# Performance work log

Hardware: AMD Instinct MI355X
Metric: run time of the kernel (lower is better)

The kernel has to match this reference:

```python
import jax, jax.numpy as jnp
from jax import lax
import numpy as np

NPOINT, K, EPS = 2048, 16, 1e-5


def fps(xyz, npoint):
    # Farthest point sampling. Deterministic start index 0 (torch uses randint).
    B, N, _ = xyz.shape
    def step(carry, _):
        distance, far = carry
        centroid = jnp.take_along_axis(xyz, far[:, None, None], axis=1)  # [B,1,3]
        d = jnp.sum((xyz - centroid) ** 2, axis=-1)                      # [B,N]
        distance = jnp.minimum(distance, d)
        return (distance, jnp.argmax(distance, axis=-1)), far
    init = (jnp.full((B, N), 1e10, dtype=xyz.dtype), jnp.zeros((B,), jnp.int32))
    _, cent = lax.scan(step, init, None, length=npoint)  # [npoint, B]
    return jnp.transpose(cent)  # [B, npoint]


def gather(points, idx):
    # points [B,N,C], idx [B,...] -> [B,...,C]
    return jax.vmap(lambda p, i: p[i])(points, idx)


def bn_relu(x, gamma, beta):
    # x [B,S,K,C]; BatchNorm2d training-mode stats over (B,S,K) per channel
    mu = jnp.mean(x, axis=(0, 1, 2), keepdims=True)
    var = jnp.var(x, axis=(0, 1, 2), keepdims=True)
    return jax.nn.relu((x - mu) * lax.rsqrt(var + EPS) * gamma + beta)


def setup_inputs() -> dict:
    key = jax.random.key(0)
    ks = jax.random.split(key, 8)
    B, N, C_in, C_out = 4, 8192, 64, 128
    return {
        'xyz': jax.random.normal(ks[0], (B, N, 3), jnp.float32),
        'feat': jax.random.normal(ks[1], (B, N, C_in), jnp.float32),
        'W1': jax.random.normal(ks[2], (C_in + 3, C_out), jnp.float32) * 0.05,
        'g1': jnp.ones((C_out,), jnp.float32),
        'b1': jnp.zeros((C_out,), jnp.float32),
        'W2': jax.random.normal(ks[3], (C_out, C_out), jnp.float32) * 0.05,
        'g2': jnp.ones((C_out,), jnp.float32),
        'b2': jnp.zeros((C_out,), jnp.float32),
    }


def reference(xyz, feat, W1, g1, b1, W2, g2, b2):
    fps_idx = fps(xyz, NPOINT)
    new_xyz = gather(xyz, fps_idx)                              # [B,S,3]
    # squared distances [B,S,N] via ||a||^2 + ||b||^2 - 2 a.b (avoids [B,S,N,3])
    d = (jnp.sum(new_xyz ** 2, -1)[:, :, None]
         + jnp.sum(xyz ** 2, -1)[:, None, :]
         - 2.0 * jnp.einsum('bsc,bnc->bsn', new_xyz, xyz))
    _, idx = lax.top_k(-d, K)                                   # [B,S,K] smallest dists
    g_xyz = gather(xyz, idx)                                    # [B,S,K,3]
    g_feat = gather(feat, idx)                                  # [B,S,K,C]
    x = jnp.concatenate([g_feat, g_xyz - new_xyz[:, :, None]], axis=-1)
    x = bn_relu(jnp.einsum('bskc,co->bsko', x, W1), g1, b1)     # 1x1 conv == matmul
    x = bn_relu(jnp.einsum('bskc,co->bsko', x, W2), g2, b2)
    new_feat = jnp.max(x, axis=2)                               # max over K -> [B,S,Cout]
    return new_xyz, new_feat
```

## Files before the change

kernel.cpp:

```cpp
#include <hip/hip_runtime.h>
#include <hip/hip_bf16.h>

#define N_PTS 8192
#define N_SAMP 2048
#define KNN_K 16
#define NBATCH 4
#define BN_M (NBATCH * N_SAMP * KNN_K)
#define NROWS (N_SAMP * NBATCH * KNN_K)
#define KNN_WAVES 2016
#define CHUNK 64

typedef float f32x2 __attribute__((ext_vector_type(2)));

template <int CTRL, int RM>
__device__ __forceinline__ unsigned umax_dpp(unsigned v) {
  unsigned o = (unsigned)__builtin_amdgcn_update_dpp((int)v, (int)v, CTRL, RM, 0xF, false);
  return (o > v) ? o : v;
}

__global__ __launch_bounds__(512) void fused_fps_knn(
    const float* __restrict__ xyz, float* __restrict__ new_xyz,
    int* __restrict__ knn_idx, int* __restrict__ progress) {
#pragma clang fp contract(off)
  __shared__ __align__(16) float xyzw[N_PTS * 4];
  __shared__ unsigned redbuf[8];
  __shared__ unsigned winslot[2];
  __shared__ int sampwin[CHUNK];
  const int tid = threadIdx.x;
  const int lane = tid & 63;

  if (blockIdx.x < NBATCH) {
    const int b = blockIdx.x;
    const int wid = tid >> 6;
    const float* base = xyz + (size_t)b * N_PTS * 3;
    for (int i = tid; i < N_PTS * 3; i += 512) {
      float v = base[i];
      int p = i / 3, c = i - p * 3;
      xyzw[p * 4 + c] = v;
    }
    for (int i = tid; i < N_PTS; i += 512) xyzw[i * 4 + 3] = 0.f;
    if (tid == 0) { winslot[0] = 0u; winslot[1] = 0xFFFFFFFFu; }
    __syncthreads();

    f32x2 px[8], py[8], pz[8], dmin[8];
#pragma unroll
    for (int j = 0; j < 8; ++j) {
      int p0 = (2 * j) * 512 + tid, p1 = p0 + 512;
      const float4 a = *reinterpret_cast<const float4*>(&xyzw[p0 * 4]);
      const float4 c = *reinterpret_cast<const float4*>(&xyzw[p1 * 4]);
      px[j] = f32x2{a.x, c.x};
      py[j] = f32x2{a.y, c.y};
      pz[j] = f32x2{a.z, c.z};
      dmin[j] = f32x2{1e10f, 1e10f};
    }
    for (int it = 1; it < N_SAMP; ++it) {
      const int p = it & 1;
      const unsigned cur = winslot[p ^ 1];
      if (tid == 0) sampwin[(it - 1) & (CHUNK - 1)] = (int)cur;
      const bool pub = (it & (CHUNK - 1)) == 0;
      if (pub && tid < CHUNK) {
        const int idx = (tid == CHUNK - 1) ? (int)cur : sampwin[tid];
        const float4 c4 = *reinterpret_cast<const float4*>(&xyzw[idx * 4]);
        float* dst = new_xyz + ((size_t)b * N_SAMP + (it - CHUNK) + tid) * 3;
        dst[0] = c4.x; dst[1] = c4.y; dst[2] = c4.z;
      }
      const float4 c4 = *reinterpret_cast<const float4*>(&xyzw[cur * 4]);
      f32x2 cX = {c4.x, c4.x}, cY = {c4.y, c4.y}, cZ = {c4.z, c4.z};
#pragma unroll
      for (int j = 0; j < 8; ++j) {
        f32x2 dx = px[j] - cX;
        f32x2 dy = py[j] - cY;
        f32x2 dz = pz[j] - cZ;
        f32x2 s01 = dx * dx + dy * dy;
        f32x2 d = s01 + dz * dz;
        dmin[j].x = fminf(dmin[j].x, d.x);
        dmin[j].y = fminf(dmin[j].y, d.y);
      }
      f32x2 m0 = {fmaxf(dmin[0].x, dmin[1].x), fmaxf(dmin[0].y, dmin[1].y)};
      f32x2 m1 = {fmaxf(dmin[2].x, dmin[3].x), fmaxf(dmin[2].y, dmin[3].y)};
      f32x2 m2 = {fmaxf(dmin[4].x, dmin[5].x), fmaxf(dmin[4].y, dmin[5].y)};
      f32x2 m3 = {fmaxf(dmin[6].x, dmin[7].x), fmaxf(dmin[6].y, dmin[7].y)};
      f32x2 n0 = {fmaxf(m0.x, m1.x), fmaxf(m0.y, m1.y)};
      f32x2 n1 = {fmaxf(m2.x, m3.x), fmaxf(m2.y, m3.y)};
      f32x2 nn = {fmaxf(n0.x, n1.x), fmaxf(n0.y, n1.y)};
      const unsigned bd = __float_as_uint(fmaxf(nn.x, nn.y));
      unsigned r = bd;
      r = umax_dpp<0xB1, 0xF>(r);
      r = umax_dpp<0x4E, 0xF>(r);
      r = umax_dpp<0x124, 0xF>(r);
      r = umax_dpp<0x128, 0xF>(r);
      r = umax_dpp<0x142, 0xA>(r);
      r = umax_dpp<0x143, 0xC>(r);
      if (lane == 63) redbuf[wid] = r;
      __syncthreads();
      if (tid == 0) {
        winslot[p ^ 1] = 0xFFFFFFFFu;
        if (pub)
          __hip_atomic_store(&progress[b], it, __ATOMIC_RELEASE, __HIP_MEMORY_SCOPE_AGENT);
      }
      unsigned g = redbuf[lane & 7];
      g = umax_dpp<0xB1, 0xF>(g);
      g = umax_dpp<0x4E, 0xF>(g);
      g = umax_dpp<0x124, 0xF>(g);
      if (bd == g) {
        unsigned cand = 0xFFFFFFFFu;
#pragma unroll
        for (int j = 7; j >= 0; --j) {
          if (__float_as_uint(dmin[j].y) == g) cand = (unsigned)((2 * j + 1) * 512 + tid);
          if (__float_as_uint(dmin[j].x) == g) cand = (unsigned)((2 * j) * 512 + tid);
        }
        atomicMin(&winslot[p], cand);
      }
      __syncthreads();
    }
    {
      const unsigned last = winslot[(N_SAMP - 1) & 1];
      if (tid < CHUNK) {
        const int idx = (tid == CHUNK - 1) ? (int)last : sampwin[tid];
        const float4 c4 = *reinterpret_cast<const float4*>(&xyzw[idx * 4]);
        float* dst = new_xyz + ((size_t)b * N_SAMP + (N_SAMP - CHUNK) + tid) * 3;
        dst[0] = c4.x; dst[1] = c4.y; dst[2] = c4.z;
      }
      __syncthreads();
      if (tid == 0)
        __hip_atomic_store(&progress[b], N_SAMP, __ATOMIC_RELEASE, __HIP_MEMORY_SCOPE_AGENT);
    }
  } else {
    const int wv = (int)(blockIdx.x - NBATCH) * 8 + (tid >> 6);
    for (int q4 = wv; q4 < NBATCH * N_SAMP; q4 += KNN_WAVES) {
      const int b = q4 & 3, s = q4 >> 2;
      while (__hip_atomic_load(&progress[b], __ATOMIC_RELAXED, __HIP_MEMORY_SCOPE_AGENT) <= s)
        __builtin_amdgcn_s_sleep(32);
      (void)__hip_atomic_load(&progress[b], __ATOMIC_ACQUIRE, __HIP_MEMORY_SCOPE_AGENT);
      const int q = b * N_SAMP + s;
      const float* qp = new_xyz + (size_t)q * 3;
      float q0 = qp[0], q1 = qp[1], q2 = qp[2];
      float qn = __fadd_rn(__fadd_rn(__fmul_rn(q0, q0), __fmul_rn(q1, q1)), __fmul_rn(q2, q2));
      const float* pb = xyz + (size_t)b * N_PTS * 3;
      unsigned long long arr[16];
#pragma unroll
      for (int i = 0; i < 16; ++i) arr[i] = ~0ull;
      for (int p = lane; p < N_PTS; p += 64) {
        float p0 = pb[p * 3 + 0], p1 = pb[p * 3 + 1], p2 = pb[p * 3 + 2];
        float pn = __fadd_rn(__fadd_rn(__fmul_rn(p0, p0), __fmul_rn(p1, p1)), __fmul_rn(p2, p2));
        float dt = fmaf(q2, p2, fmaf(q1, p1, __fmul_rn(q0, p0)));
        float d = __fsub_rn(__fadd_rn(qn, pn), __fmul_rn(2.0f, dt));
        unsigned ub = __float_as_uint(d);
        ub ^= (unsigned)((int)ub >> 31) | 0x80000000u;
        unsigned long long key = ((unsigned long long)ub << 32) | (unsigned)p;
        if (key < arr[15]) {
          unsigned long long curk = key;
#pragma unroll
          for (int j = 0; j < 16; ++j) {
            unsigned long long lo = (curk < arr[j]) ? curk : arr[j];
            unsigned long long hi = (curk < arr[j]) ? arr[j] : curk;
            arr[j] = lo; curk = hi;
          }
        }
      }
      for (int r = 0; r < KNN_K; ++r) {
        unsigned long long m = arr[0];
#pragma unroll
        for (int o = 32; o > 0; o >>= 1) {
          unsigned long long other = __shfl_xor(m, o, 64);
          m = (other < m) ? other : m;
        }
        if (arr[0] == m) {
#pragma unroll
          for (int j = 0; j < 15; ++j) arr[j] = arr[j + 1];
          arr[15] = ~0ull;
        }
        if (lane == r) knn_idx[(size_t)q * KNN_K + r] = (int)(m & 0xFFFFFFFFu);
      }
    }
  }
}

__global__ __launch_bounds__(256) void gemm1_kernel(
    const float* __restrict__ xyz, const float* __restrict__ feat,
    const float* __restrict__ W1, const float* __restrict__ new_xyz,
    const int* __restrict__ knn_i, float* __restrict__ y1, float* __restrict__ stats1) {
  __shared__ __align__(16) float At[67 * 128];
  __shared__ __align__(16) float Wq[17 * 128];
  __shared__ float part[4 * 256];
  __shared__ int nb[128];
  const int t = threadIdx.x, blk = blockIdx.x;
  const int row0 = blk * 128;
  if (t < 128) nb[t] = knn_i[row0 + t];
  __syncthreads();
  {
    const int r = t >> 1, q = t & 1;
    const int rg = row0 + r, bs = rg >> 4, b = bs >> 11;
    const float* fr = feat + ((size_t)b * N_PTS + nb[r]) * 64 + q * 32;
#pragma unroll
    for (int i = 0; i < 8; ++i) {
      float4 v = *reinterpret_cast<const float4*>(fr + 4 * i);
      int c = q * 32 + 4 * i;
      At[(c + 0) * 128 + r] = v.x; At[(c + 1) * 128 + r] = v.y;
      At[(c + 2) * 128 + r] = v.z; At[(c + 3) * 128 + r] = v.w;
    }
    if (q == 0) {
      const float* pr = xyz + ((size_t)b * N_PTS + nb[r]) * 3;
      const float* qr = new_xyz + (size_t)bs * 3;
      At[64 * 128 + r] = pr[0] - qr[0];
      At[65 * 128 + r] = pr[1] - qr[1];
      At[66 * 128 + r] = pr[2] - qr[2];
    }
  }
  float acc[8][8];
#pragma unroll
  for (int i = 0; i < 8; ++i)
#pragma unroll
    for (int j = 0; j < 8; ++j) acc[i][j] = 0.f;
  const int ry = t >> 4, cx = t & 15;
  for (int kq = 0; kq < 4; ++kq) {
    const int kbase = kq * 17;
    const int nk = (67 - kbase) < 17 ? (67 - kbase) : 17;
    __syncthreads();
    for (int i = t; i < nk * 32; i += 256)
      reinterpret_cast<float4*>(Wq)[i] =
          reinterpret_cast<const float4*>(W1 + (size_t)kbase * 128)[i];
    __syncthreads();
    for (int kk = 0; kk < nk; ++kk) {
      const float4 a0 = *reinterpret_cast<const float4*>(&At[(kbase + kk) * 128 + ry * 8]);
      const float4 a1 = *reinterpret_cast<const float4*>(&At[(kbase + kk) * 128 + ry * 8 + 4]);
      const float4 w0 = *reinterpret_cast<const float4*>(&Wq[kk * 128 + cx * 8]);
      const float4 w1 = *reinterpret_cast<const float4*>(&Wq[kk * 128 + cx * 8 + 4]);
      const float a[8] = {a0.x, a0.y, a0.z, a0.w, a1.x, a1.y, a1.z, a1.w};
      const float w[8] = {w0.x, w0.y, w0.z, w0.w, w1.x, w1.y, w1.z, w1.w};
#pragma unroll
      for (int i = 0; i < 8; ++i)
#pragma unroll
        for (int j = 0; j < 8; ++j) acc[i][j] = fmaf(a[i], w[j], acc[i][j]);
    }
  }
#pragma unroll
  for (int i = 0; i < 8; ++i) {
    float4 v0 = {acc[i][0], acc[i][1], acc[i][2], acc[i][3]};
    float4 v1 = {acc[i][4], acc[i][5], acc[i][6], acc[i][7]};
    float* dst = y1 + ((size_t)row0 + ry * 8 + i) * 128 + cx * 8;
    *reinterpret_cast<float4*>(dst) = v0;
    *reinterpret_cast<float4*>(dst + 4) = v1;
  }
  float s8[8], q8[8];
#pragma unroll
  for (int j = 0; j < 8; ++j) {
    s8[j] = 0.f; q8[j] = 0.f;
#pragma unroll
    for (int i = 0; i < 8; ++i) { s8[j] += acc[i][j]; q8[j] += acc[i][j] * acc[i][j]; }
  }
#pragma unroll
  for (int j = 0; j < 8; ++j) {
    s8[j] += __shfl_xor(s8[j], 16, 64); q8[j] += __shfl_xor(q8[j], 16, 64);
    s8[j] += __shfl_xor(s8[j], 32, 64); q8[j] += __shfl_xor(q8[j], 32, 64);
  }
  const int w = t >> 6, lane = t & 63;
  if (lane < 16) {
#pragma unroll
    for (int j = 0; j < 8; ++j) {
      part[w * 256 + lane * 8 + j] = s8[j];
      part[w * 256 + 128 + lane * 8 + j] = q8[j];
    }
  }
  __syncthreads();
  {
    int ch = t & 127, which = t >> 7;
    float v = part[0 * 256 + which * 128 + ch] + part[1 * 256 + which * 128 + ch] +
              part[2 * 256 + which * 128 + ch] + part[3 * 256 + which * 128 + ch];
    atomicAdd(&stats1[which * 128 + ch], v);
  }
}

__global__ __launch_bounds__(256) void gemm2_kernel(
    const float* __restrict__ y1, const float* __restrict__ W2,
    const float* __restrict__ stats1, const float* __restrict__ g1v,
    const float* __restrict__ b1v, float* __restrict__ y2, float* __restrict__ stats2) {
  __shared__ __align__(16) float Ah[64 * 128];
  __shared__ __align__(16) float Wq[32 * 128];
  __shared__ float part[4 * 256];
  __shared__ float s1[128], h1[128];
  const int t = threadIdx.x, blk = blockIdx.x;
  const int row0 = blk * 128;
  const float inv_m = 1.0f / (float)BN_M;
  if (t < 128) {
    float m = stats1[t] * inv_m;
    float var = stats1[128 + t] * inv_m - m * m;
    float rs = rsqrtf(var + 1e-5f);
    float sc = rs * g1v[t];
    s1[t] = sc;
    h1[t] = b1v[t] - m * sc;
  }
  float acc[8][8];
#pragma unroll
  for (int i = 0; i < 8; ++i)
#pragma unroll
    for (int j = 0; j < 8; ++j) acc[i][j] = 0.f;
  const int ry = t >> 4, cx = t & 15;
  for (int kh = 0; kh < 2; ++kh) {
    __syncthreads();
    {
      const int r = t >> 1, q = t & 1;
      const float* src = y1 + ((size_t)row0 + r) * 128 + kh * 64 + q * 32;
#pragma unroll
      for (int i = 0; i < 8; ++i) {
        float4 v = *reinterpret_cast<const float4*>(src + 4 * i);
        int c = kh * 64 + q * 32 + 4 * i;
        int cl = c - kh * 64;
        Ah[(cl + 0) * 128 + r] = fmaxf(fmaf(v.x, s1[c + 0], h1[c + 0]), 0.f);
        Ah[(cl + 1) * 128 + r] = fmaxf(fmaf(v.y, s1[c + 1], h1[c + 1]), 0.f);
        Ah[(cl + 2) * 128 + r] = fmaxf(fmaf(v.z, s1[c + 2], h1[c + 2]), 0.f);
        Ah[(cl + 3) * 128 + r] = fmaxf(fmaf(v.w, s1[c + 3], h1[c + 3]), 0.f);
      }
    }
    for (int kq = 0; kq < 2; ++kq) {
      __syncthreads();
      const int kbase = kh * 64 + kq * 32;
      for (int i = t; i < 32 * 32; i += 256)
        reinterpret_cast<float4*>(Wq)[i] =
            reinterpret_cast<const float4*>(W2 + (size_t)kbase * 128)[i];
      __syncthreads();
      for (int kk = 0; kk < 32; ++kk) {
        const int kl = kq * 32 + kk;
        const float4 a0 = *reinterpret_cast<const float4*>(&Ah[kl * 128 + ry * 8]);
        const float4 a1 = *reinterpret_cast<const float4*>(&Ah[kl * 128 + ry * 8 + 4]);
        const float4 w0 = *reinterpret_cast<const float4*>(&Wq[kk * 128 + cx * 8]);
        const float4 w1 = *reinterpret_cast<const float4*>(&Wq[kk * 128 + cx * 8 + 4]);
        const float a[8] = {a0.x, a0.y, a0.z, a0.w, a1.x, a1.y, a1.z, a1.w};
        const float w[8] = {w0.x, w0.y, w0.z, w0.w, w1.x, w1.y, w1.z, w1.w};
#pragma unroll
        for (int i = 0; i < 8; ++i)
#pragma unroll
          for (int j = 0; j < 8; ++j) acc[i][j] = fmaf(a[i], w[j], acc[i][j]);
      }
    }
  }
#pragma unroll
  for (int i = 0; i < 8; ++i) {
    float4 v0 = {acc[i][0], acc[i][1], acc[i][2], acc[i][3]};
    float4 v1 = {acc[i][4], acc[i][5], acc[i][6], acc[i][7]};
    float* dst = y2 + ((size_t)row0 + ry * 8 + i) * 128 + cx * 8;
    *reinterpret_cast<float4*>(dst) = v0;
    *reinterpret_cast<float4*>(dst + 4) = v1;
  }
  float s8[8], q8[8];
#pragma unroll
  for (int j = 0; j < 8; ++j) {
    s8[j] = 0.f; q8[j] = 0.f;
#pragma unroll
    for (int i = 0; i < 8; ++i) { s8[j] += acc[i][j]; q8[j] += acc[i][j] * acc[i][j]; }
  }
#pragma unroll
  for (int j = 0; j < 8; ++j) {
    s8[j] += __shfl_xor(s8[j], 16, 64); q8[j] += __shfl_xor(q8[j], 16, 64);
    s8[j] += __shfl_xor(s8[j], 32, 64); q8[j] += __shfl_xor(q8[j], 32, 64);
  }
  const int w = t >> 6, lane = t & 63;
  if (lane < 16) {
#pragma unroll
    for (int j = 0; j < 8; ++j) {
      part[w * 256 + lane * 8 + j] = s8[j];
      part[w * 256 + 128 + lane * 8 + j] = q8[j];
    }
  }
  __syncthreads();
  {
    int ch = t & 127, which = t >> 7;
    float v = part[0 * 256 + which * 128 + ch] + part[1 * 256 + which * 128 + ch] +
              part[2 * 256 + which * 128 + ch] + part[3 * 256 + which * 128 + ch];
    atomicAdd(&stats2[which * 128 + ch], v);
  }
}

__global__ __launch_bounds__(256) void pool_kernel(
    const float* __restrict__ y2, const float* __restrict__ stats2,
    const float* __restrict__ g2v, const float* __restrict__ b2v,
    float* __restrict__ out_feat) {
  __shared__ float s2[128], h2[128];
  __shared__ float part[4 * 128];
  const int t = threadIdx.x, blk = blockIdx.x;
  const float inv_m = 1.0f / (float)BN_M;
  if (t < 128) {
    float m = stats2[t] * inv_m;
    float var = stats2[128 + t] * inv_m - m * m;
    float rs = rsqrtf(var + 1e-5f);
    float sc = rs * g2v[t];
    s2[t] = sc;
    h2[t] = b2v[t] - m * sc;
  }
  __syncthreads();
  const int c4 = (t & 31) * 4, rg = t >> 5;
  const int lane = t & 63, w = t >> 6;
  for (int s = 0; s < 8; ++s) {
    const int bs = blk * 8 + s;
    float4 m4 = {-1e30f, -1e30f, -1e30f, -1e30f};
#pragma unroll
    for (int rr = 0; rr < 2; ++rr) {
      const int r = bs * 16 + rg * 2 + rr;
      float4 v = *reinterpret_cast<const float4*>(y2 + (size_t)r * 128 + c4);
      float4 z = {fmaxf(fmaf(v.x, s2[c4 + 0], h2[c4 + 0]), 0.f),
                  fmaxf(fmaf(v.y, s2[c4 + 1], h2[c4 + 1]), 0.f),
                  fmaxf(fmaf(v.z, s2[c4 + 2], h2[c4 + 2]), 0.f),
                  fmaxf(fmaf(v.w, s2[c4 + 3], h2[c4 + 3]), 0.f)};
      m4.x = fmaxf(m4.x, z.x); m4.y = fmaxf(m4.y, z.y);
      m4.z = fmaxf(m4.z, z.z); m4.w = fmaxf(m4.w, z.w);
    }
    m4.x = fmaxf(m4.x, __shfl_xor(m4.x, 32, 64));
    m4.y = fmaxf(m4.y, __shfl_xor(m4.y, 32, 64));
    m4.z = fmaxf(m4.z, __shfl_xor(m4.z, 32, 64));
    m4.w = fmaxf(m4.w, __shfl_xor(m4.w, 32, 64));
    if (lane < 32) {
      part[w * 128 + c4 + 0] = m4.x; part[w * 128 + c4 + 1] = m4.y;
      part[w * 128 + c4 + 2] = m4.z; part[w * 128 + c4 + 3] = m4.w;
    }
    __syncthreads();
    if (t < 128) {
      float mm = fmaxf(fmaxf(part[t], part[128 + t]), fmaxf(part[256 + t], part[384 + t]));
      out_feat[(size_t)bs * 128 + t] = mm;
    }
    __syncthreads();
  }
}

extern "C" void kernel_launch(void* const* d_in, const int* in_sizes, int n_in,
                              void* d_out, int out_size, void* d_ws, size_t ws_size,
                              hipStream_t stream) {
  const float* xyz  = (const float*)d_in[0];
  const float* feat = (const float*)d_in[1];
  const float* W1   = (const float*)d_in[2];
  const float* g1   = (const float*)d_in[3];
  const float* b1   = (const float*)d_in[4];
  const float* W2   = (const float*)d_in[5];
  const float* g2   = (const float*)d_in[6];
  const float* b2   = (const float*)d_in[7];
  float* out = (float*)d_out;
  float* new_xyz = out;
  float* out_feat = out + NBATCH * N_SAMP * 3;

  int* fps_i = (int*)d_ws;
  int* knn_i = fps_i + NBATCH * N_SAMP;
  float* stats1 = (float*)(knn_i + NROWS);
  float* stats2 = stats1 + 256;
  int* progress = (int*)(stats2 + 256);
  float* y1 = (float*)(progress + 64);
  float* y2 = y1 + (size_t)NROWS * 128;

  hipMemsetAsync(stats1, 0, (256 + 256 + 64) * sizeof(float), stream);
  hipLaunchKernelGGL(fused_fps_knn, dim3(NBATCH + 252), dim3(512), 0, stream,
                     xyz, new_xyz, knn_i, progress);
  hipLaunchKernelGGL(gemm1_kernel, dim3(NROWS / 128), dim3(256), 0, stream,
                     xyz, feat, W1, new_xyz, knn_i, y1, stats1);
  hipLaunchKernelGGL(gemm2_kernel, dim3(NROWS / 128), dim3(256), 0, stream,
                     y1, W2, stats1, g1, b1, y2, stats2);
  hipLaunchKernelGGL(pool_kernel, dim3(NBATCH * N_SAMP / 8), dim3(256), 0, stream,
                     y2, stats2, g2, b2, out_feat);
}
```

Baseline: 2.078 ms.

## Reduce GEMM2 output to per-sample max/min and apply BN sign-aware in pool

Instead of writing the full pre-BN y2 tensor and re-reading it in the pool kernel, gemm2 now reduces each sample's 16 neighbor rows to per-channel max and min in registers and writes only those. The pool kernel applies the affine BN plus ReLU to max or min depending on the sign of the scale, which is exact because BN is monotonic per channel. This removes a large global write and read of y2. It also enlarges the FPS chunk size and lengthens the KNN spin-wait sleep, which change the FPS/KNN handoff granularity and polling behaviour.

```diff
diff --git a/kernel.cpp b/kernel.cpp
--- a/kernel.cpp
+++ b/kernel.cpp
@@ -8,7 +8,7 @@
 #define BN_M (NBATCH * N_SAMP * KNN_K)
 #define NROWS (N_SAMP * NBATCH * KNN_K)
 #define KNN_WAVES 2016
-#define CHUNK 64
+#define CHUNK 128
 
 typedef float f32x2 __attribute__((ext_vector_type(2)));
 
@@ -130,7 +130,7 @@
     for (int q4 = wv; q4 < NBATCH * N_SAMP; q4 += KNN_WAVES) {
       const int b = q4 & 3, s = q4 >> 2;
       while (__hip_atomic_load(&progress[b], __ATOMIC_RELAXED, __HIP_MEMORY_SCOPE_AGENT) <= s)
-        __builtin_amdgcn_s_sleep(32);
+        __builtin_amdgcn_s_sleep(64);
       (void)__hip_atomic_load(&progress[b], __ATOMIC_ACQUIRE, __HIP_MEMORY_SCOPE_AGENT);
       const int q = b * N_SAMP + s;
       const float* qp = new_xyz + (size_t)q * 3;
@@ -274,7 +274,8 @@
 __global__ __launch_bounds__(256) void gemm2_kernel(
     const float* __restrict__ y1, const float* __restrict__ W2,
     const float* __restrict__ stats1, const float* __restrict__ g1v,
-    const float* __restrict__ b1v, float* __restrict__ y2, float* __restrict__ stats2) {
+    const float* __restrict__ b1v, float* __restrict__ ymax, float* __restrict__ ymin,
+    float* __restrict__ stats2) {
   __shared__ __align__(16) float Ah[64 * 128];
   __shared__ __align__(16) float Wq[32 * 128];
   __shared__ float part[4 * 256];
@@ -334,13 +335,29 @@
       }
     }
   }
-#pragma unroll
-  for (int i = 0; i < 8; ++i) {
-    float4 v0 = {acc[i][0], acc[i][1], acc[i][2], acc[i][3]};
-    float4 v1 = {acc[i][4], acc[i][5], acc[i][6], acc[i][7]};
-    float* dst = y2 + ((size_t)row0 + ry * 8 + i) * 128 + cx * 8;
-    *reinterpret_cast<float4*>(dst) = v0;
-    *reinterpret_cast<float4*>(dst + 4) = v1;
+  float mx[8], mn[8];
+#pragma unroll
+  for (int j = 0; j < 8; ++j) { mx[j] = acc[0][j]; mn[j] = acc[0][j]; }
+#pragma unroll
+  for (int i = 1; i < 8; ++i)
+#pragma unroll
+    for (int j = 0; j < 8; ++j) {
+      mx[j] = fmaxf(mx[j], acc[i][j]);
+      mn[j] = fminf(mn[j], acc[i][j]);
+    }
+#pragma unroll
+  for (int j = 0; j < 8; ++j) {
+    mx[j] = fmaxf(mx[j], __shfl_xor(mx[j], 16, 64));
+    mn[j] = fminf(mn[j], __shfl_xor(mn[j], 16, 64));
+  }
+  if ((ry & 1) == 0) {
+    const int smp = blk * 8 + (ry >> 1);
+    float4 a0 = {mx[0], mx[1], mx[2], mx[3]}, a1 = {mx[4], mx[5], mx[6], mx[7]};
+    float4 b0 = {mn[0], mn[1], mn[2], mn[3]}, b1 = {mn[4], mn[5], mn[6], mn[7]};
+    float* dm = ymax + (size_t)smp * 128 + cx * 8;
+    *reinterpret_cast<float4*>(dm) = a0; *reinterpret_cast<float4*>(dm + 4) = a1;
+    float* dn = ymin + (size_t)smp * 128 + cx * 8;
+    *reinterpret_cast<float4*>(dn) = b0; *reinterpret_cast<float4*>(dn + 4) = b1;
   }
   float s8[8], q8[8];
 #pragma unroll
@@ -372,53 +389,19 @@
 }
 
 __global__ __launch_bounds__(256) void pool_kernel(
-    const float* __restrict__ y2, const float* __restrict__ stats2,
-    const float* __restrict__ g2v, const float* __restrict__ b2v,
-    float* __restrict__ out_feat) {
-  __shared__ float s2[128], h2[128];
-  __shared__ float part[4 * 128];
-  const int t = threadIdx.x, blk = blockIdx.x;
+    const float* __restrict__ ymax, const float* __restrict__ ymin,
+    const float* __restrict__ stats2, const float* __restrict__ g2v,
+    const float* __restrict__ b2v, float* __restrict__ out_feat) {
+  const int idx = blockIdx.x * 256 + threadIdx.x;
+  const int ch = idx & 127;
   const float inv_m = 1.0f / (float)BN_M;
-  if (t < 128) {
-    float m = stats2[t] * inv_m;
-    float var = stats2[128 + t] * inv_m - m * m;
-    float rs = rsqrtf(var + 1e-5f);
-    float sc = rs * g2v[t];
-    s2[t] = sc;
-    h2[t] = b2v[t] - m * sc;
-  }
-  __syncthreads();
-  const int c4 = (t & 31) * 4, rg = t >> 5;
-  const int lane = t & 63, w = t >> 6;
-  for (int s = 0; s < 8; ++s) {
-    const int bs = blk * 8 + s;
-    float4 m4 = {-1e30f, -1e30f, -1e30f, -1e30f};
-#pragma unroll
-    for (int rr = 0; rr < 2; ++rr) {
-      const int r = bs * 16 + rg * 2 + rr;
-      float4 v = *reinterpret_cast<const float4*>(y2 + (size_t)r * 128 + c4);
-      float4 z = {fmaxf(fmaf(v.x, s2[c4 + 0], h2[c4 + 0]), 0.f),
-                  fmaxf(fmaf(v.y, s2[c4 + 1], h2[c4 + 1]), 0.f),
-                  fmaxf(fmaf(v.z, s2[c4 + 2], h2[c4 + 2]), 0.f),
-                  fmaxf(fmaf(v.w, s2[c4 + 3], h2[c4 + 3]), 0.f)};
-      m4.x = fmaxf(m4.x, z.x); m4.y = fmaxf(m4.y, z.y);
-      m4.z = fmaxf(m4.z, z.z); m4.w = fmaxf(m4.w, z.w);
-    }
-    m4.x = fmaxf(m4.x, __shfl_xor(m4.x, 32, 64));
-    m4.y = fmaxf(m4.y, __shfl_xor(m4.y, 32, 64));
-    m4.z = fmaxf(m4.z, __shfl_xor(m4.z, 32, 64));
-    m4.w = fmaxf(m4.w, __shfl_xor(m4.w, 32, 64));
-    if (lane < 32) {
-      part[w * 128 + c4 + 0] = m4.x; part[w * 128 + c4 + 1] = m4.y;
-      part[w * 128 + c4 + 2] = m4.z; part[w * 128 + c4 + 3] = m4.w;
-    }
-    __syncthreads();
-    if (t < 128) {
-      float mm = fmaxf(fmaxf(part[t], part[128 + t]), fmaxf(part[256 + t], part[384 + t]));
-      out_feat[(size_t)bs * 128 + t] = mm;
-    }
-    __syncthreads();
-  }
+  float m = stats2[ch] * inv_m;
+  float var = stats2[128 + ch] * inv_m - m * m;
+  float rs = rsqrtf(var + 1e-5f);
+  float sc = rs * g2v[ch];
+  float h = b2v[ch] - m * sc;
+  float v = (sc > 0.f) ? ymax[idx] : ymin[idx];
+  out_feat[idx] = fmaxf(fmaf(v, sc, h), 0.f);
 }
 
 extern "C" void kernel_launch(void* const* d_in, const int* in_sizes, int n_in,
@@ -442,7 +425,8 @@
   float* stats2 = stats1 + 256;
   int* progress = (int*)(stats2 + 256);
   float* y1 = (float*)(progress + 64);
-  float* y2 = y1 + (size_t)NROWS * 128;
+  float* ymax = y1 + (size_t)NROWS * 128;
+  float* ymin = ymax + (size_t)NBATCH * N_SAMP * 128;
 
   hipMemsetAsync(stats1, 0, (256 + 256 + 64) * sizeof(float), stream);
   hipLaunchKernelGGL(fused_fps_knn, dim3(NBATCH + 252), dim3(512), 0, stream,
@@ -450,7 +434,7 @@
   hipLaunchKernelGGL(gemm1_kernel, dim3(NROWS / 128), dim3(256), 0, stream,
                      xyz, feat, W1, new_xyz, knn_i, y1, stats1);
   hipLaunchKernelGGL(gemm2_kernel, dim3(NROWS / 128), dim3(256), 0, stream,
-                     y1, W2, stats1, g1, b1, y2, stats2);
-  hipLaunchKernelGGL(pool_kernel, dim3(NBATCH * N_SAMP / 8), dim3(256), 0, stream,
-                     y2, stats2, g2, b2, out_feat);
-}
+                     y1, W2, stats1, g1, b1, ymax, ymin, stats2);
+  hipLaunchKernelGGL(pool_kernel, dim3(NBATCH * N_SAMP * 128 / 256), dim3(256), 0, stream,
+                     ymax, ymin, stats2, g2, b2, out_feat);
+}
```

After: 2.039 ms, median of 2. Within noise of the previous version (-1.9%).
